# Kernel tuning notes

Hardware: AMD Instinct MI355X
Metric: run time of the kernel (lower is better)

Reference implementation:

```python
import jax, jax.numpy as jnp
import numpy as np

NUM_HEADS = 12
HEAD_DIM = 64
HIDDEN = NUM_HEADS * HEAD_DIM
AGENT_NUM = 40
MAX_POS = 2048
SCALE = HEAD_DIM ** -0.5


def _split_heads(x):
    # [b, s, hidden] -> [b, h, s, d]
    b, s, _ = x.shape
    return x.reshape(b, s, NUM_HEADS, HEAD_DIM).transpose(0, 2, 1, 3)


def _agent_pool(q, agent_num):
    # F.interpolate(q[None], size=(agent_num, dim), mode='bilinear', align_corners=False)
    # width (dim) is unchanged so it reduces to 1D linear interp along seq axis.
    b, s, dim = q.shape
    src = (jnp.arange(agent_num, dtype=q.dtype) + 0.5) * (s / agent_num) - 0.5
    src = jnp.clip(src, 0.0, s - 1.0)
    lo = jnp.floor(src).astype(jnp.int32)
    hi = jnp.minimum(lo + 1, s - 1)
    w = (src - lo.astype(q.dtype))[None, :, None]  # [1, A, 1]
    return q[:, lo, :] * (1.0 - w) + q[:, hi, :] * w  # [b, A, dim]


def setup_inputs() -> dict:
    key = jax.random.key(0)
    ks = jax.random.split(key, 6)
    bs, S = 16, 2048
    return {
        "hidden_states": jax.random.normal(ks[0], (bs, S, HIDDEN), jnp.float32),
        "attention_mask": jnp.zeros((bs, 1, 1, S), jnp.float32),
        "Wq": jax.random.normal(ks[1], (HIDDEN, HIDDEN), jnp.float32) * 0.02,
        "bq": jnp.zeros((HIDDEN,), jnp.float32),
        "Wk": jax.random.normal(ks[2], (HIDDEN, HIDDEN), jnp.float32) * 0.02,
        "bk": jnp.zeros((HIDDEN,), jnp.float32),
        "Wv": jax.random.normal(ks[3], (HIDDEN, HIDDEN), jnp.float32) * 0.02,
        "bv": jnp.zeros((HIDDEN,), jnp.float32),
        "dist_emb": jax.random.normal(ks[4], (2 * MAX_POS - 1, HEAD_DIM), jnp.float32) * 0.02,
    }


def reference(hidden_states, attention_mask, Wq, bq, Wk, bk, Wv, bv, dist_emb):
    bs, S, dim = hidden_states.shape
    q = hidden_states @ Wq + bq          # [b, S, hidden] (== query_layer flattened back)
    k = hidden_states @ Wk + bk
    v = hidden_states @ Wv + bv
    q_layer = _split_heads(q)            # [b, h, S, d]
    k_layer = _split_heads(k)
    v_layer = _split_heads(v)

    agent = _agent_pool(q, AGENT_NUM)    # [b, A, hidden]
    agent_layer = _split_heads(agent)    # [b, h, A, d]

    # stage 1: agent -> KV, with relative-key position bias
    d1 = jnp.arange(AGENT_NUM)[:, None] - jnp.arange(S)[None, :] + (MAX_POS - 1)
    pe1 = dist_emb[d1]                   # [A, S, d]
    bias1 = jnp.einsum('bhad,asd->bhas', agent_layer, pe1)
    score1 = jnp.einsum('bhad,bhsd->bhas', agent_layer * SCALE, k_layer) + bias1
    score1 = score1 + attention_mask     # [b,1,1,S] broadcasts over (h, A)
    p1 = jax.nn.softmax(score1, axis=-1)
    agent_v = jnp.einsum('bhas,bhsd->bhad', p1, v_layer)  # [b, h, A, d]

    # stage 2: query -> agents, with relative-key position bias
    d2 = jnp.arange(S)[:, None] - jnp.arange(AGENT_NUM)[None, :] + (MAX_POS - 1)
    pe2 = dist_emb[d2]                   # [S, A, d]
    bias2 = jnp.einsum('bhsd,sad->bhsa', q_layer, pe2)
    score2 = jnp.einsum('bhsd,bhad->bhsa', q_layer * SCALE, agent_layer) + bias2
    q_mask = jnp.swapaxes(attention_mask, -1, -2)  # [b,1,S,1]
    score2 = score2 + q_mask
    p2 = jax.nn.softmax(score2, axis=-1)
    x = jnp.einsum('bhsa,bhad->bhsd', p2, agent_v)  # [b, h, S, d]
    return x.transpose(0, 2, 1, 3).reshape(bs, S, dim)
```

## Files before the change

kernel.cpp:

```cpp
#include <hip/hip_runtime.h>
#include <math.h>

#define B_ 16
#define S_ 2048
#define H_ 12
#define D_ 64
#define HID 768
#define A_ 40
#define SCALE_ 0.125f
#define CH1 8
#define SUBT 64
#define NSUB 4

typedef __attribute__((ext_vector_type(8))) short short8v;
typedef __attribute__((ext_vector_type(4))) float f32x4;
typedef __attribute__((ext_vector_type(16))) float f32x16;

__device__ __forceinline__ unsigned f2bf_bits(float x) {
    unsigned u = __float_as_uint(x);
    return (u + 0x7FFFu + ((u >> 16) & 1u)) >> 16;
}

__device__ __forceinline__ void split1(float v, unsigned short& h, unsigned short& l) {
    __bf16 bh = (__bf16)v;
    float hf = (float)bh;
    __bf16 bl = (__bf16)(v - hf);
    h = __builtin_bit_cast(unsigned short, bh);
    l = __builtin_bit_cast(unsigned short, bl);
}

__device__ __forceinline__ void split8c(const float* x, int4& hi, int4& lo) {
    unsigned h[8], l[8];
#pragma unroll
    for (int i = 0; i < 8; i++) {
        __bf16 bh = (__bf16)x[i];
        float hf = (float)bh;
        __bf16 bl = (__bf16)(x[i] - hf);
        h[i] = (unsigned)__builtin_bit_cast(unsigned short, bh);
        l[i] = (unsigned)__builtin_bit_cast(unsigned short, bl);
    }
    hi = make_int4((int)(h[0] | (h[1] << 16)), (int)(h[2] | (h[3] << 16)),
                   (int)(h[4] | (h[5] << 16)), (int)(h[6] | (h[7] << 16)));
    lo = make_int4((int)(l[0] | (l[1] << 16)), (int)(l[2] | (l[3] << 16)),
                   (int)(l[4] | (l[5] << 16)), (int)(l[6] | (l[7] << 16)));
}

__global__ void wt_convert(const float* __restrict__ Wq, const float* __restrict__ Wk,
                           const float* __restrict__ Wv,
                           unsigned short* __restrict__ Wth, unsigned short* __restrict__ Wtl)
{
    int idx = blockIdx.x * 256 + threadIdx.x;
    if (idx >= 3 * 192 * 768) return;
    int n  = idx % 768;
    int kc = (idx / 768) % 192;
    int z  = idx / (768 * 192);
    const float* W = (z == 0) ? Wq : (z == 1) ? Wk : Wv;
    unsigned short h4[4], l4[4];
#pragma unroll
    for (int i = 0; i < 4; i++) {
        float x = W[(size_t)(4 * kc + i) * HID + n];
        unsigned hb = f2bf_bits(x);
        float hf = __uint_as_float(hb << 16);
        h4[i] = (unsigned short)hb;
        l4[i] = (unsigned short)f2bf_bits(x - hf);
    }
    size_t o = ((size_t)z * HID + n) * HID + 4 * kc;
    *(ushort4*)&Wth[o] = make_ushort4(h4[0], h4[1], h4[2], h4[3]);
    *(ushort4*)&Wtl[o] = make_ushort4(l4[0], l4[1], l4[2], l4[3]);
}

__global__ void dist_frag(const float* __restrict__ dist,
                          unsigned short* __restrict__ DFh, unsigned short* __restrict__ DFl)
{
    int g = blockIdx.x * 256 + threadIdx.x;
    if (g >= 256 * 2 * 64) return;
    int lane = g & 63;
    int ks = (g >> 6) & 1;
    int u  = g >> 7;
    int row = 8 + u * 16 + (lane & 15);
    int col = ks * 32 + ((lane >> 4) << 3);
    float xv[8];
#pragma unroll
    for (int j = 0; j < 8; j++)
        xv[j] = (row < 4095) ? dist[(size_t)row * D_ + col + j] : 0.f;
    int4 hi, lo;
    split8c(xv, hi, lo);
    *(int4*)&DFh[(size_t)g * 8] = hi;
    *(int4*)&DFl[(size_t)g * 8] = lo;
}

__global__ void ag_frag(const float* __restrict__ Ag,
                        unsigned short* __restrict__ Gh, unsigned short* __restrict__ Gl)
{
    int g = blockIdx.x * 256 + threadIdx.x;
    if (g >= 192 * 3 * 2 * 64) return;
    int lane = g & 63;
    int r = g >> 6;
    int ks = r & 1; r >>= 1;
    int at = r % 3;
    int bh = r / 3;
    int a = at * 16 + (lane & 15);
    int col = ks * 32 + ((lane >> 4) << 3);
    float xv[8];
#pragma unroll
    for (int j = 0; j < 8; j++)
        xv[j] = (a < A_) ? SCALE_ * Ag[((size_t)bh * A_ + a) * D_ + col + j] : 0.f;
    int4 hi, lo;
    split8c(xv, hi, lo);
    *(int4*)&Gh[(size_t)g * 8] = hi;
    *(int4*)&Gl[(size_t)g * 8] = lo;
}

__global__ void avt_frag(const float* __restrict__ AgV,
                         unsigned short* __restrict__ Vh, unsigned short* __restrict__ Vl)
{
    int g = blockIdx.x * 256 + threadIdx.x;
    if (g >= 192 * 4 * 2 * 64) return;
    int lane = g & 63;
    int r = g >> 6;
    int ks = r & 1; r >>= 1;
    int nt = r & 3;
    int bh = r >> 2;
    int d = nt * 16 + (lane & 15);
    int a0 = ks * 32 + ((lane >> 4) << 3);
    float xv[8];
#pragma unroll
    for (int j = 0; j < 8; j++) {
        int a = a0 + j;
        xv[j] = (a < A_) ? AgV[((size_t)bh * A_ + a) * D_ + d] : 0.f;
    }
    int4 hi, lo;
    split8c(xv, hi, lo);
    *(int4*)&Vh[(size_t)g * 8] = hi;
    *(int4*)&Vl[(size_t)g * 8] = lo;
}

__global__ __launch_bounds__(512, 2) void qkv_z(
    const float* __restrict__ X,
    const unsigned short* __restrict__ Wth, const unsigned short* __restrict__ Wtl,
    const float* __restrict__ bq, const float* __restrict__ bk, const float* __restrict__ bv,
    float* __restrict__ Q, float* __restrict__ K, float* __restrict__ V)
{
    const int L   = blockIdx.x;
    const int k8  = L & 7, sl_ = L >> 3;
    const int mt  = k8 * 32 + sl_ / 9;
    const int sub = sl_ % 9;
    const int nt  = sub % 3, zz = sub / 3;
    const int m0 = mt * 128, n0 = nt * 256;

    const float* __restrict__ bias = (zz == 0) ? bq : (zz == 1) ? bk : bv;
    float* __restrict__ Out        = (zz == 0) ? Q  : (zz == 1) ? K  : V;
    const unsigned short* __restrict__ Bhg = Wth + (size_t)zz * HID * HID;
    const unsigned short* __restrict__ Blg = Wtl + (size_t)zz * HID * HID;

    __shared__ unsigned short Ah[128][40];
    __shared__ unsigned short Al[128][40];
    __shared__ unsigned short Bh[256][40];
    __shared__ unsigned short Bl[256][40];

    const int t = threadIdx.x;
    const int lane = t & 63, w = t >> 6;
    const int wm = (w & 1) * 64, wn = (w >> 1) * 64;
    const int r32 = lane & 31, kh = lane >> 5;

    const int sr = t >> 2, sca = (t & 3) * 8;
    const int sb = t >> 1, scb = (t & 1) * 16;

    f32x16 acc[2][2];
#pragma unroll
    for (int i = 0; i < 2; i++)
#pragma unroll
        for (int j = 0; j < 2; j++)
#pragma unroll
            for (int p = 0; p < 16; p++) acc[i][j][p] = 0.f;

    for (int k0 = 0; k0 < HID; k0 += 32) {
        float xv[8];
        const float* xp = X + (size_t)(m0 + sr) * HID + k0 + sca;
        float4 f0 = *(const float4*)xp;
        float4 f1 = *(const float4*)(xp + 4);
        xv[0] = f0.x; xv[1] = f0.y; xv[2] = f0.z; xv[3] = f0.w;
        xv[4] = f1.x; xv[5] = f1.y; xv[6] = f1.z; xv[7] = f1.w;
        int4 ah, al;
        split8c(xv, ah, al);
        size_t bo = (size_t)(n0 + sb) * HID + k0 + scb;
        int4 bh0 = *(const int4*)&Bhg[bo];
        int4 bh1 = *(const int4*)&Bhg[bo + 8];
        int4 bl0 = *(const int4*)&Blg[bo];
        int4 bl1 = *(const int4*)&Blg[bo + 8];

        __syncthreads();
        *(int4*)&Ah[sr][sca] = ah;
        *(int4*)&Al[sr][sca] = al;
        *(int4*)&Bh[sb][scb]     = bh0;  *(int4*)&Bh[sb][scb + 8] = bh1;
        *(int4*)&Bl[sb][scb]     = bl0;  *(int4*)&Bl[sb][scb + 8] = bl1;
        __syncthreads();

#pragma unroll
        for (int ks = 0; ks < 2; ks++) {
            const int ko = ks * 16 + kh * 8;
            short8v a_h[2], a_l[2], b_h[2], b_l[2];
#pragma unroll
            for (int i = 0; i < 2; i++) {
                a_h[i] = *(const short8v*)&Ah[wm + i * 32 + r32][ko];
                a_l[i] = *(const short8v*)&Al[wm + i * 32 + r32][ko];
                b_h[i] = *(const short8v*)&Bh[wn + i * 32 + r32][ko];
                b_l[i] = *(const short8v*)&Bl[wn + i * 32 + r32][ko];
            }
#pragma unroll
            for (int i = 0; i < 2; i++)
#pragma unroll
                for (int j = 0; j < 2; j++) {
                    acc[i][j] = __builtin_amdgcn_mfma_f32_32x32x16_bf16(a_h[i], b_h[j], acc[i][j], 0, 0, 0);
                    acc[i][j] = __builtin_amdgcn_mfma_f32_32x32x16_bf16(a_l[i], b_h[j], acc[i][j], 0, 0, 0);
                    acc[i][j] = __builtin_amdgcn_mfma_f32_32x32x16_bf16(a_h[i], b_l[j], acc[i][j], 0, 0, 0);
                }
        }
    }

    const float scl = (zz == 1) ? SCALE_ : 1.0f;
#pragma unroll
    for (int j = 0; j < 2; j++) {
        int n = n0 + wn + j * 32 + r32;
        float bj = bias[n];
        int h = n >> 6, d = n & 63;
#pragma unroll
        for (int i = 0; i < 2; i++) {
#pragma unroll
            for (int p = 0; p < 16; p++) {
                int m = m0 + wm + i * 32 + (p & 3) + 8 * (p >> 2) + 4 * kh;
                int b = m >> 11, s = m & 2047;
                Out[(((size_t)b * H_ + h) * S_ + s) * D_ + d] = (acc[i][j][p] + bj) * scl;
            }
        }
    }
}

__global__ void agent_pool(const float* __restrict__ Q, float* __restrict__ Ag)
{
    int idx = blockIdx.x * 256 + threadIdx.x;
    if (idx >= B_ * H_ * A_ * D_) return;
    int d  = idx & 63;
    int a  = (idx >> 6) % A_;
    int bh = idx / (A_ * D_);
    float src = ((float)a + 0.5f) * (2048.0f / 40.0f) - 0.5f;
    src = fminf(fmaxf(src, 0.0f), 2047.0f);
    int lo = (int)floorf(src);
    int hi = min(lo + 1, S_ - 1);
    float w = src - (float)lo;
    const float* base = Q + (size_t)bh * (S_ * D_);
    Ag[idx] = base[lo * D_ + d] * (1.0f - w) + base[hi * D_ + d] * w;
}

__global__ __launch_bounds__(256, 3) void stage1_part(
    const float* __restrict__ Kl, const float* __restrict__ Vl,
    const float* __restrict__ Ag, const float* __restrict__ dist,
    const float* __restrict__ mask,
    float* __restrict__ Pacc, float* __restrict__ Pm, float* __restrict__ Pl)
{
    const int q  = blockIdx.x;
    const int bh = blockIdx.y;
    const int b  = bh / H_;
    const int s0 = q * (NSUB * SUBT);
    const float* __restrict__ kb = Kl + (size_t)bh * (S_ * D_);
    const float* __restrict__ vb = Vl + (size_t)bh * (S_ * D_);

    __shared__ float ag[A_][D_];
    __shared__ float pv[103 * 68];
    __shared__ float sc[SUBT][44];
    __shared__ float pm6[6][A_];
    __shared__ float mrow[A_], lrow[A_], resc[A_];

    const int t  = threadIdx.x;
    const int sl = t >> 2, dq = t & 3;

    for (int i = t; i < A_ * D_ / 4; i += 256)
        ((float4*)ag)[i] = ((const float4*)(Ag + (size_t)bh * (A_ * D_)))[i];
    if (t < A_) { mrow[t] = -INFINITY; lrow[t] = 0.0f; }

    float4 acc[3];
#pragma unroll
    for (int ii = 0; ii < 3; ii++) acc[ii] = make_float4(0.f, 0.f, 0.f, 0.f);

    for (int st = 0; st < NSUB; st++) {
        const int sb = s0 + st * SUBT;
        const int jbase = 1984 - sb;

        __syncthreads();
        for (int i = t; i < 103 * 16; i += 256) {
            int r = i >> 4, c = i & 15;
            *(float4*)&pv[r * 68 + c * 4] = *(const float4*)&dist[(size_t)(jbase + r) * D_ + c * 4];
        }
        const int s = sb + sl;
        float4 kreg[4];
        const float* kp = kb + (size_t)s * D_ + dq * 16;
#pragma unroll
        for (int c = 0; c < 4; c++) kreg[c] = *(const float4*)(kp + 4 * c);
        float mval = mask[(size_t)b * S_ + s];
        __syncthreads();

        for (int a = 0; a < A_; a++) {
            const float* per = &pv[(a + 63 - sl) * 68 + dq * 16];
            const float* agr = &ag[a][dq * 16];
            float sum = 0.0f;
#pragma unroll
            for (int c = 0; c < 4; c++) {
                float4 p4 = *(const float4*)(per + 4 * c);
                float4 a4 = *(const float4*)(agr + 4 * c);
                float4 k4 = kreg[c];
                sum = fmaf(a4.x, k4.x + p4.x, sum);
                sum = fmaf(a4.y, k4.y + p4.y, sum);
                sum = fmaf(a4.z, k4.z + p4.z, sum);
                sum = fmaf(a4.w, k4.w + p4.w, sum);
            }
            sum += __shfl_xor(sum, 1);
            sum += __shfl_xor(sum, 2);
            if (dq == 0) sc[sl][a] = sum + mval;
        }
        __syncthreads();

        for (int i = t; i < SUBT * 16; i += 256) {
            int r = i >> 4, c = i & 15;
            *(float4*)&pv[r * 68 + c * 4] = *(const float4*)&vb[(size_t)(sb + r) * D_ + c * 4];
        }
        if (t < 240) {
            int a = t % 40, r6 = t / 40;
            float mx = -INFINITY;
            for (int i = r6; i < SUBT; i += 6) mx = fmaxf(mx, sc[i][a]);
            pm6[r6][a] = mx;
        }
        __syncthreads();
        if (t < A_) {
            float lm = pm6[0][t];
#pragma unroll
            for (int r6 = 1; r6 < 6; r6++) lm = fmaxf(lm, pm6[r6][t]);
            float mnew = fmaxf(mrow[t], lm);
            resc[t] = __expf(mrow[t] - mnew);
            mrow[t] = mnew;
        }
        __syncthreads();
        for (int i = t; i < SUBT * A_; i += 256) {
            int rr = i / 40, aa = i - rr * 40;
            sc[rr][aa] = __expf(sc[rr][aa] - mrow[aa]);
        }
        __syncthreads();
        if (t < 240) {
            int a = t % 40, r6 = t / 40;
            float sm = 0.0f;
            for (int i = r6; i < SUBT; i += 6) sm += sc[i][a];
            pm6[r6][a] = sm;
        }
        __syncthreads();
        if (t < A_) {
            float ls = pm6[0][t] + pm6[1][t] + pm6[2][t] + pm6[3][t] + pm6[4][t] + pm6[5][t];
            lrow[t] = lrow[t] * resc[t] + ls;
        }

#pragma unroll
        for (int ii = 0; ii < 3; ii++) {
            int i = t + ii * 256;
            if (i < A_ * 16) {
                int a = i >> 4, d4 = i & 15;
                float rs = resc[a];
                float4 c4 = acc[ii];
                c4.x *= rs; c4.y *= rs; c4.z *= rs; c4.w *= rs;
                for (int rr = 0; rr < SUBT; rr++) {
                    float p = sc[rr][a];
                    float4 v4 = *(const float4*)&pv[rr * 68 + d4 * 4];
                    c4.x = fmaf(p, v4.x, c4.x);
                    c4.y = fmaf(p, v4.y, c4.y);
                    c4.z = fmaf(p, v4.z, c4.z);
                    c4.w = fmaf(p, v4.w, c4.w);
                }
                acc[ii] = c4;
            }
        }
    }
    __syncthreads();
#pragma unroll
    for (int ii = 0; ii < 3; ii++) {
        int i = t + ii * 256;
        if (i < A_ * 16) {
            int a = i >> 4, d4 = i & 15;
            *(float4*)&Pacc[(((size_t)(bh * CH1 + q) * A_) + a) * D_ + d4 * 4] = acc[ii];
        }
    }
    if (t < A_) {
        Pm[(size_t)(bh * CH1 + q) * A_ + t] = mrow[t];
        Pl[(size_t)(bh * CH1 + q) * A_ + t] = lrow[t];
    }
}

__global__ __launch_bounds__(256) void stage1_reduce(
    const float* __restrict__ Pacc, const float* __restrict__ Pm,
    const float* __restrict__ Pl, float* __restrict__ AgV)
{
    const int bh = blockIdx.x;
    const int t = threadIdx.x;
    __shared__ float F[CH1][A_], Linv[A_];
    if (t < A_) {
        float M = -INFINITY;
#pragma unroll
        for (int q = 0; q < CH1; q++) M = fmaxf(M, Pm[(size_t)(bh * CH1 + q) * A_ + t]);
        float L = 0.0f;
#pragma unroll
        for (int q = 0; q < CH1; q++) {
            float f = __expf(Pm[(size_t)(bh * CH1 + q) * A_ + t] - M);
            F[q][t] = f;
            L = fmaf(f, Pl[(size_t)(bh * CH1 + q) * A_ + t], L);
        }
        Linv[t] = 1.0f / L;
    }
    __syncthreads();
#pragma unroll
    for (int ii = 0; ii < 3; ii++) {
        int i = t + ii * 256;
        if (i < A_ * 16) {
            int a = i >> 4, d4 = i & 15;
            float4 s4 = make_float4(0.f, 0.f, 0.f, 0.f);
            for (int q = 0; q < CH1; q++) {
                float f = F[q][a];
                float4 p4 = *(const float4*)&Pacc[(((size_t)(bh * CH1 + q) * A_) + a) * D_ + d4 * 4];
                s4.x = fmaf(f, p4.x, s4.x);
                s4.y = fmaf(f, p4.y, s4.y);
                s4.z = fmaf(f, p4.z, s4.z);
                s4.w = fmaf(f, p4.w, s4.w);
            }
            float inv = Linv[a];
            s4.x *= inv; s4.y *= inv; s4.z *= inv; s4.w *= inv;
            *(float4*)&AgV[(size_t)bh * (A_ * D_) + a * D_ + d4 * 4] = s4;
        }
    }
}

__global__ __launch_bounds__(256, 2) void stage2_mfma(
    const float* __restrict__ Qg,
    const unsigned short* __restrict__ AGFh, const unsigned short* __restrict__ AGFl,
    const unsigned short* __restrict__ DFh,  const unsigned short* __restrict__ DFl,
    const unsigned short* __restrict__ AVFh, const unsigned short* __restrict__ AVFl,
    float* __restrict__ Out)
{
    const int sbk = blockIdx.x;
    const int bh  = blockIdx.y;
    const int b = bh / H_, h = bh % H_;
    const int s0 = sbk * 64;
    const int base_u = 4 * sbk + 125;

    __shared__ unsigned short Qfh[8 * 64 * 8], Qfl[8 * 64 * 8];
    __shared__ float scm[64][52];
    __shared__ float scp[64][68];
    __shared__ unsigned short PAh[64][72], PAl[64][72];

    const int t = threadIdx.x;
    const int lane = t & 63, ts = t >> 6;
    const int fr = lane & 15, kg = lane >> 4;

    {
        const int r = t >> 2, c0 = (t & 3) * 16;
        const float* qp = Qg + ((size_t)bh * S_ + s0 + r) * D_ + c0;
        float xa[8], xb[8];
        float4 f0 = *(const float4*)(qp);
        float4 f1 = *(const float4*)(qp + 4);
        float4 f2 = *(const float4*)(qp + 8);
        float4 f3 = *(const float4*)(qp + 12);
        xa[0]=f0.x; xa[1]=f0.y; xa[2]=f0.z; xa[3]=f0.w;
        xa[4]=f1.x; xa[5]=f1.y; xa[6]=f1.z; xa[7]=f1.w;
        xb[0]=f2.x; xb[1]=f2.y; xb[2]=f2.z; xb[3]=f2.w;
        xb[4]=f3.x; xb[5]=f3.y; xb[6]=f3.z; xb[7]=f3.w;
        int4 h0, l0, h1, l1;
        split8c(xa, h0, l0);
        split8c(xb, h1, l1);
        const int tsr = r >> 4, frr = r & 15;
        const int c8a = (t & 3) * 2, c8b = c8a + 1;
        const int oa = ((tsr * 2 + (c8a >> 2)) * 64 + (((c8a & 3) << 4) | frr)) * 8;
        const int ob = ((tsr * 2 + (c8b >> 2)) * 64 + (((c8b & 3) << 4) | frr)) * 8;
        *(int4*)&Qfh[oa] = h0;  *(int4*)&Qfl[oa] = l0;
        *(int4*)&Qfh[ob] = h1;  *(int4*)&Qfl[ob] = l1;
    }
    __syncthreads();

    short8v qh[2], ql[2];
#pragma unroll
    for (int ks = 0; ks < 2; ks++) {
        qh[ks] = *(const short8v*)&Qfh[((ts * 2 + ks) * 64 + lane) * 8];
        ql[ks] = *(const short8v*)&Qfl[((ts * 2 + ks) * 64 + lane) * 8];
    }

#pragma unroll
    for (int at = 0; at < 3; at++) {
        f32x4 acc = (f32x4){0.f, 0.f, 0.f, 0.f};
#pragma unroll
        for (int ks = 0; ks < 2; ks++) {
            size_t o = ((((size_t)bh * 3 + at) * 2 + ks) * 64 + lane) * 8;
            short8v chv = *(const short8v*)&AGFh[o];
            short8v clv = *(const short8v*)&AGFl[o];
            acc = __builtin_amdgcn_mfma_f32_16x16x32_bf16(chv, qh[ks], acc, 0, 0, 0);
            acc = __builtin_amdgcn_mfma_f32_16x16x32_bf16(clv, qh[ks], acc, 0, 0, 0);
            acc = __builtin_amdgcn_mfma_f32_16x16x32_bf16(chv, ql[ks], acc, 0, 0, 0);
        }
        *(f32x4*)&scm[ts * 16 + fr][at * 16 + kg * 4] = acc;
    }
#pragma unroll
    for (int o4 = 0; o4 < 4; o4++) {
        f32x4 acc = (f32x4){0.f, 0.f, 0.f, 0.f};
        const int u = base_u + ts + o4;
#pragma unroll
        for (int ks = 0; ks < 2; ks++) {
            size_t o = (((size_t)u * 2 + ks) * 64 + lane) * 8;
            short8v chv = *(const short8v*)&DFh[o];
            short8v clv = *(const short8v*)&DFl[o];
            acc = __builtin_amdgcn_mfma_f32_16x16x32_bf16(chv, qh[ks], acc, 0, 0, 0);
            acc = __builtin_amdgcn_mfma_f32_16x16x32_bf16(clv, qh[ks], acc, 0, 0, 0);
            acc = __builtin_amdgcn_mfma_f32_16x16x32_bf16(chv, ql[ks], acc, 0, 0, 0);
        }
        *(f32x4*)&scp[ts * 16 + fr][o4 * 16 + kg * 4] = acc;
    }
    __syncthreads();

    {
        const int r = t >> 2, dq = t & 3;
        const int base = (r & 15) + 39;
        float val[10];
#pragma unroll
        for (int i = 0; i < 10; i++) {
            int a = dq * 10 + i;
            val[i] = scm[r][a] + scp[r][base - a];
        }
        float mx = -INFINITY;
#pragma unroll
        for (int i = 0; i < 10; i++) mx = fmaxf(mx, val[i]);
        mx = fmaxf(mx, __shfl_xor(mx, 1));
        mx = fmaxf(mx, __shfl_xor(mx, 2));
        float sum = 0.f;
#pragma unroll
        for (int i = 0; i < 10; i++) { val[i] = __expf(val[i] - mx); sum += val[i]; }
        sum += __shfl_xor(sum, 1);
        sum += __shfl_xor(sum, 2);
        float inv = 1.0f / sum;
        unsigned* ph = (unsigned*)&PAh[r][0];
        unsigned* pl = (unsigned*)&PAl[r][0];
#pragma unroll
        for (int i = 0; i < 5; i++) {
            unsigned short h0, l0, h1, l1;
            split1(val[2 * i] * inv, h0, l0);
            split1(val[2 * i + 1] * inv, h1, l1);
            ph[dq * 5 + i] = (unsigned)h0 | ((unsigned)h1 << 16);
            pl[dq * 5 + i] = (unsigned)l0 | ((unsigned)l1 << 16);
        }
#pragma unroll
        for (int i = 0; i < 3; i++) { ph[20 + dq * 3 + i] = 0u; pl[20 + dq * 3 + i] = 0u; }
    }
    __syncthreads();

    short8v ph8[2], pl8[2];
#pragma unroll
    for (int ks = 0; ks < 2; ks++) {
        ph8[ks] = *(const short8v*)&PAh[ts * 16 + fr][ks * 32 + kg * 8];
        pl8[ks] = *(const short8v*)&PAl[ts * 16 + fr][ks * 32 + kg * 8];
    }
#pragma unroll
    for (int nt = 0; nt < 4; nt++) {
        f32x4 acc = (f32x4){0.f, 0.f, 0.f, 0.f};
#pragma unroll
        for (int ks = 0; ks < 2; ks++) {
            size_t o = ((((size_t)bh * 4 + nt) * 2 + ks) * 64 + lane) * 8;
            short8v vh = *(const short8v*)&AVFh[o];
            short8v vl = *(const short8v*)&AVFl[o];
            acc = __builtin_amdgcn_mfma_f32_16x16x32_bf16(ph8[ks], vh, acc, 0, 0, 0);
            acc = __builtin_amdgcn_mfma_f32_16x16x32_bf16(pl8[ks], vh, acc, 0, 0, 0);
            acc = __builtin_amdgcn_mfma_f32_16x16x32_bf16(ph8[ks], vl, acc, 0, 0, 0);
        }
        const int d = nt * 16 + fr;
        float* op = Out + ((size_t)b * S_ + s0 + ts * 16 + kg * 4) * HID + h * D_ + d;
#pragma unroll
        for (int r = 0; r < 4; r++)
            op[(size_t)r * HID] = acc[r];
    }
}

extern "C" void kernel_launch(void* const* d_in, const int* in_sizes, int n_in,
                              void* d_out, int out_size, void* d_ws, size_t ws_size,
                              hipStream_t stream) {
    const float* hs   = (const float*)d_in[0];
    const float* mask = (const float*)d_in[1];
    const float* Wq   = (const float*)d_in[2];
    const float* bq   = (const float*)d_in[3];
    const float* Wk   = (const float*)d_in[4];
    const float* bk   = (const float*)d_in[5];
    const float* Wv   = (const float*)d_in[6];
    const float* bv   = (const float*)d_in[7];
    const float* dist = (const float*)d_in[8];
    float* out = (float*)d_out;

    float* ws = (float*)d_ws;
    const size_t QKV = (size_t)B_ * H_ * S_ * D_;
    const size_t AG  = (size_t)B_ * H_ * A_ * D_;
    float* Q     = ws;
    float* K     = ws + QKV;
    float* V     = ws + 2 * QKV;
    float* Agent = ws + 3 * QKV;
    float* AgV   = Agent + AG;
    float* Pacc  = AgV + AG;
    float* Pm    = Pacc + (size_t)B_ * H_ * CH1 * A_ * D_;
    float* Pl    = Pm + (size_t)B_ * H_ * CH1 * A_;
    unsigned short* Wth = (unsigned short*)(Pl + (size_t)B_ * H_ * CH1 * A_);
    unsigned short* Wtl = Wth + (size_t)3 * HID * HID;
    unsigned short* DFh = Wtl + (size_t)3 * HID * HID;
    unsigned short* DFl = DFh + (size_t)262144;
    unsigned short* AGFh = DFl + (size_t)262144;
    unsigned short* AGFl = AGFh + (size_t)589824;
    unsigned short* AVFh = AGFl + (size_t)589824;
    unsigned short* AVFl = AVFh + (size_t)786432;

    wt_convert<<<(3 * 192 * 768 + 255) / 256, 256, 0, stream>>>(Wq, Wk, Wv, Wth, Wtl);
    dist_frag<<<(256 * 2 * 64 + 255) / 256, 256, 0, stream>>>(dist, DFh, DFl);
    qkv_z<<<2304, 512, 0, stream>>>(hs, Wth, Wtl, bq, bk, bv, Q, K, V);
    agent_pool<<<(B_ * H_ * A_ * D_ + 255) / 256, 256, 0, stream>>>(Q, Agent);
    ag_frag<<<(192 * 3 * 2 * 64 + 255) / 256, 256, 0, stream>>>(Agent, AGFh, AGFl);
    dim3 g1(CH1, B_ * H_);
    stage1_part<<<g1, 256, 0, stream>>>(K, V, Agent, dist, mask, Pacc, Pm, Pl);
    stage1_reduce<<<B_ * H_, 256, 0, stream>>>(Pacc, Pm, Pl, AgV);
    avt_frag<<<(192 * 4 * 2 * 64 + 255) / 256, 256, 0, stream>>>(AgV, AVFh, AVFl);
    dim3 g2(32, B_ * H_);
    stage2_mfma<<<g2, 256, 0, stream>>>(Q, AGFh, AGFl, DFh, DFl, AVFh, AVFl, out);
}
```

Before: 654.4 us.

## Move stage-1 agent attention onto bf16x3 MFMA with split QK and position-bias GEMMs

Rewrites the stage-1 kernel so the agent·K score, the agent·dist_emb position bias, and the P·V accumulation all run on 16x16x32 bf16 MFMA using a hi/lo split (three products) to keep near-fp32 accuracy. The position bias is computed as a small dense GEMM over a 112-row band of dist_emb and then diagonally gathered, instead of per-element dot products. New fragment-conversion kernels (dist_frag0, an unscaled ag_frag) are launched and K/V tiles are converted to bf16 fragments in shared memory each subtile. This adds conversion overhead, more shared memory and lower occupancy (launch bound 2) in exchange for replacing scalar FMA loops with matrix instructions.

```diff
diff --git a/kernel.cpp b/kernel.cpp
--- a/kernel.cpp
+++ b/kernel.cpp
@@ -89,8 +89,28 @@
     *(int4*)&DFl[(size_t)g * 8] = lo;
 }
 
+__global__ void dist_frag0(const float* __restrict__ dist,
+                           unsigned short* __restrict__ Dh, unsigned short* __restrict__ Dl)
+{
+    int g = blockIdx.x * 256 + threadIdx.x;
+    if (g >= 131 * 2 * 64) return;
+    int lane = g & 63;
+    int ks = (g >> 6) & 1;
+    int u  = g >> 7;
+    int row = u * 16 + (lane & 15);
+    int col = ks * 32 + ((lane >> 4) << 3);
+    float xv[8];
+#pragma unroll
+    for (int j = 0; j < 8; j++) xv[j] = dist[(size_t)row * D_ + col + j];
+    int4 hi, lo;
+    split8c(xv, hi, lo);
+    *(int4*)&Dh[(size_t)g * 8] = hi;
+    *(int4*)&Dl[(size_t)g * 8] = lo;
+}
+
 __global__ void ag_frag(const float* __restrict__ Ag,
-                        unsigned short* __restrict__ Gh, unsigned short* __restrict__ Gl)
+                        unsigned short* __restrict__ Gh, unsigned short* __restrict__ Gl,
+                        float scale)
 {
     int g = blockIdx.x * 256 + threadIdx.x;
     if (g >= 192 * 3 * 2 * 64) return;
@@ -104,7 +124,7 @@
     float xv[8];
 #pragma unroll
     for (int j = 0; j < 8; j++)
-        xv[j] = (a < A_) ? SCALE_ * Ag[((size_t)bh * A_ + a) * D_ + col + j] : 0.f;
+        xv[j] = (a < A_) ? scale * Ag[((size_t)bh * A_ + a) * D_ + col + j] : 0.f;
     int4 hi, lo;
     split8c(xv, hi, lo);
     *(int4*)&Gh[(size_t)g * 8] = hi;
@@ -252,9 +272,10 @@
     Ag[idx] = base[lo * D_ + d] * (1.0f - w) + base[hi * D_ + d] * w;
 }
 
-__global__ __launch_bounds__(256, 3) void stage1_part(
+__global__ __launch_bounds__(256, 2) void stage1_mfma(
     const float* __restrict__ Kl, const float* __restrict__ Vl,
-    const float* __restrict__ Ag, const float* __restrict__ dist,
+    const unsigned short* __restrict__ AG1h, const unsigned short* __restrict__ AG1l,
+    const unsigned short* __restrict__ D0h,  const unsigned short* __restrict__ D0l,
     const float* __restrict__ mask,
     float* __restrict__ Pacc, float* __restrict__ Pm, float* __restrict__ Pl)
 {
@@ -265,64 +286,122 @@
     const float* __restrict__ kb = Kl + (size_t)bh * (S_ * D_);
     const float* __restrict__ vb = Vl + (size_t)bh * (S_ * D_);
 
-    __shared__ float ag[A_][D_];
-    __shared__ float pv[103 * 68];
-    __shared__ float sc[SUBT][44];
+    __shared__ unsigned short KFh[4096], KFl[4096];
+    __shared__ unsigned short VTh[4096], VTl[4096];
+    __shared__ float sc[SUBT][52];
+    __shared__ float scp[112][52];
     __shared__ float pm6[6][A_];
-    __shared__ float mrow[A_], lrow[A_], resc[A_];
-
-    const int t  = threadIdx.x;
-    const int sl = t >> 2, dq = t & 3;
-
-    for (int i = t; i < A_ * D_ / 4; i += 256)
-        ((float4*)ag)[i] = ((const float4*)(Ag + (size_t)bh * (A_ * D_)))[i];
+    __shared__ float mrow[A_], lrow[A_], resc[A_], mrw[SUBT];
+
+    const int t = threadIdx.x;
+    const int lane = t & 63, w = t >> 6;
+    const int fr = lane & 15, kg = lane >> 4;
+
     if (t < A_) { mrow[t] = -INFINITY; lrow[t] = 0.0f; }
 
-    float4 acc[3];
-#pragma unroll
-    for (int ii = 0; ii < 3; ii++) acc[ii] = make_float4(0.f, 0.f, 0.f, 0.f);
+    f32x4 acc3[3];
+#pragma unroll
+    for (int at = 0; at < 3; at++) acc3[at] = (f32x4){0.f, 0.f, 0.f, 0.f};
 
     for (int st = 0; st < NSUB; st++) {
         const int sb = s0 + st * SUBT;
-        const int jbase = 1984 - sb;
-
-        __syncthreads();
-        for (int i = t; i < 103 * 16; i += 256) {
-            int r = i >> 4, c = i & 15;
-            *(float4*)&pv[r * 68 + c * 4] = *(const float4*)&dist[(size_t)(jbase + r) * D_ + c * 4];
-        }
-        const int s = sb + sl;
-        float4 kreg[4];
-        const float* kp = kb + (size_t)s * D_ + dq * 16;
-#pragma unroll
-        for (int c = 0; c < 4; c++) kreg[c] = *(const float4*)(kp + 4 * c);
-        float mval = mask[(size_t)b * S_ + s];
-        __syncthreads();
-
-        for (int a = 0; a < A_; a++) {
-            const float* per = &pv[(a + 63 - sl) * 68 + dq * 16];
-            const float* agr = &ag[a][dq * 16];
-            float sum = 0.0f;
-#pragma unroll
-            for (int c = 0; c < 4; c++) {
-                float4 p4 = *(const float4*)(per + 4 * c);
-                float4 a4 = *(const float4*)(agr + 4 * c);
-                float4 k4 = kreg[c];
-                sum = fmaf(a4.x, k4.x + p4.x, sum);
-                sum = fmaf(a4.y, k4.y + p4.y, sum);
-                sum = fmaf(a4.z, k4.z + p4.z, sum);
-                sum = fmaf(a4.w, k4.w + p4.w, sum);
+        const int u0 = (1984 - sb) >> 4;
+
+        __syncthreads();
+
+        {
+            const int r = t >> 2, c0 = (t & 3) * 16;
+            const float* kp = kb + (size_t)(sb + r) * D_ + c0;
+            float xa[8], xb[8];
+            float4 f0 = *(const float4*)(kp);
+            float4 f1 = *(const float4*)(kp + 4);
+            float4 f2 = *(const float4*)(kp + 8);
+            float4 f3 = *(const float4*)(kp + 12);
+            xa[0]=f0.x; xa[1]=f0.y; xa[2]=f0.z; xa[3]=f0.w;
+            xa[4]=f1.x; xa[5]=f1.y; xa[6]=f1.z; xa[7]=f1.w;
+            xb[0]=f2.x; xb[1]=f2.y; xb[2]=f2.z; xb[3]=f2.w;
+            xb[4]=f3.x; xb[5]=f3.y; xb[6]=f3.z; xb[7]=f3.w;
+            int4 h0, l0, h1, l1;
+            split8c(xa, h0, l0);
+            split8c(xb, h1, l1);
+            const int tsr = r >> 4, frr = r & 15;
+            const int c8a = (t & 3) * 2, c8b = c8a + 1;
+            const int oa = ((tsr * 2 + (c8a >> 2)) * 64 + (((c8a & 3) << 4) | frr)) * 8;
+            const int ob = ((tsr * 2 + (c8b >> 2)) * 64 + (((c8b & 3) << 4) | frr)) * 8;
+            *(int4*)&KFh[oa] = h0;  *(int4*)&KFl[oa] = l0;
+            *(int4*)&KFh[ob] = h1;  *(int4*)&KFl[ob] = l1;
+        }
+        {
+            const int r = t >> 2, c0 = (t & 3) * 16;
+            const float* vp = vb + (size_t)(sb + r) * D_ + c0;
+            float vv[16];
+            float4 g0 = *(const float4*)(vp);
+            float4 g1 = *(const float4*)(vp + 4);
+            float4 g2 = *(const float4*)(vp + 8);
+            float4 g3 = *(const float4*)(vp + 12);
+            vv[0]=g0.x; vv[1]=g0.y; vv[2]=g0.z; vv[3]=g0.w;
+            vv[4]=g1.x; vv[5]=g1.y; vv[6]=g1.z; vv[7]=g1.w;
+            vv[8]=g2.x; vv[9]=g2.y; vv[10]=g2.z; vv[11]=g2.w;
+            vv[12]=g3.x; vv[13]=g3.y; vv[14]=g3.z; vv[15]=g3.w;
+            const int ks2 = r >> 5, kgp = (r & 31) >> 3, e = r & 7;
+#pragma unroll
+            for (int jj = 0; jj < 16; jj++) {
+                int d = c0 + jj;
+                int off = (((d >> 4) * 2 + ks2) * 64 + kgp * 16 + (d & 15)) * 8 + e;
+                unsigned short h, l;
+                split1(vv[jj], h, l);
+                VTh[off] = h; VTl[off] = l;
             }
-            sum += __shfl_xor(sum, 1);
-            sum += __shfl_xor(sum, 2);
-            if (dq == 0) sc[sl][a] = sum + mval;
-        }
-        __syncthreads();
-
-        for (int i = t; i < SUBT * 16; i += 256) {
-            int r = i >> 4, c = i & 15;
-            *(float4*)&pv[r * 68 + c * 4] = *(const float4*)&vb[(size_t)(sb + r) * D_ + c * 4];
-        }
+        }
+        if (t < SUBT) mrw[t] = mask[(size_t)b * S_ + sb + t];
+        __syncthreads();
+
+        {
+            const int ts = w;
+#pragma unroll
+            for (int at = 0; at < 3; at++) {
+                f32x4 a4 = (f32x4){0.f, 0.f, 0.f, 0.f};
+#pragma unroll
+                for (int ks = 0; ks < 2; ks++) {
+                    size_t oA = ((((size_t)bh * 3 + at) * 2 + ks) * 64 + lane) * 8;
+                    short8v gh = *(const short8v*)&AG1h[oA];
+                    short8v gl = *(const short8v*)&AG1l[oA];
+                    short8v kh2 = *(const short8v*)&KFh[((ts * 2 + ks) * 64 + lane) * 8];
+                    short8v kl2 = *(const short8v*)&KFl[((ts * 2 + ks) * 64 + lane) * 8];
+                    a4 = __builtin_amdgcn_mfma_f32_16x16x32_bf16(gh, kh2, a4, 0, 0, 0);
+                    a4 = __builtin_amdgcn_mfma_f32_16x16x32_bf16(gl, kh2, a4, 0, 0, 0);
+                    a4 = __builtin_amdgcn_mfma_f32_16x16x32_bf16(gh, kl2, a4, 0, 0, 0);
+                }
+                *(f32x4*)&sc[ts * 16 + fr][at * 16 + kg * 4] = a4;
+            }
+        }
+        for (int ut = w; ut < 7; ut += 4) {
+            const int u = u0 + ut;
+#pragma unroll
+            for (int at = 0; at < 3; at++) {
+                f32x4 a4 = (f32x4){0.f, 0.f, 0.f, 0.f};
+#pragma unroll
+                for (int ks = 0; ks < 2; ks++) {
+                    size_t oA = ((((size_t)bh * 3 + at) * 2 + ks) * 64 + lane) * 8;
+                    short8v gh = *(const short8v*)&AG1h[oA];
+                    short8v gl = *(const short8v*)&AG1l[oA];
+                    size_t oD = (((size_t)u * 2 + ks) * 64 + lane) * 8;
+                    short8v dh = *(const short8v*)&D0h[oD];
+                    short8v dl = *(const short8v*)&D0l[oD];
+                    a4 = __builtin_amdgcn_mfma_f32_16x16x32_bf16(gh, dh, a4, 0, 0, 0);
+                    a4 = __builtin_amdgcn_mfma_f32_16x16x32_bf16(gl, dh, a4, 0, 0, 0);
+                    a4 = __builtin_amdgcn_mfma_f32_16x16x32_bf16(gh, dl, a4, 0, 0, 0);
+                }
+                *(f32x4*)&scp[ut * 16 + fr][at * 16 + kg * 4] = a4;
+            }
+        }
+        __syncthreads();
+
+        for (int i = t; i < SUBT * A_; i += 256) {
+            int rr = i / 40, aa = i - rr * 40;
+            sc[rr][aa] += scp[aa + 63 - rr][aa] + mrw[rr];
+        }
+        __syncthreads();
         if (t < 240) {
             int a = t % 40, r6 = t / 40;
             float mx = -INFINITY;
@@ -355,34 +434,62 @@
             float ls = pm6[0][t] + pm6[1][t] + pm6[2][t] + pm6[3][t] + pm6[4][t] + pm6[5][t];
             lrow[t] = lrow[t] * resc[t] + ls;
         }
-
-#pragma unroll
-        for (int ii = 0; ii < 3; ii++) {
-            int i = t + ii * 256;
-            if (i < A_ * 16) {
-                int a = i >> 4, d4 = i & 15;
-                float rs = resc[a];
-                float4 c4 = acc[ii];
-                c4.x *= rs; c4.y *= rs; c4.z *= rs; c4.w *= rs;
-                for (int rr = 0; rr < SUBT; rr++) {
-                    float p = sc[rr][a];
-                    float4 v4 = *(const float4*)&pv[rr * 68 + d4 * 4];
-                    c4.x = fmaf(p, v4.x, c4.x);
-                    c4.y = fmaf(p, v4.y, c4.y);
-                    c4.z = fmaf(p, v4.z, c4.z);
-                    c4.w = fmaf(p, v4.w, c4.w);
+        __syncthreads();
+
+        for (int g = t; g < 384; g += 256) {
+            int pl = g & 63;
+            int c = g >> 6;
+            int at = c >> 1, ks2 = c & 1;
+            int a = at * 16 + (pl & 15);
+            int sl0 = ks2 * 32 + (pl >> 4) * 8;
+            float xv[8];
+#pragma unroll
+            for (int e = 0; e < 8; e++)
+                xv[e] = (a < A_) ? sc[sl0 + e][a] : 0.f;
+            int4 hi, lo;
+            split8c(xv, hi, lo);
+            *(int4*)&KFh[g * 8] = hi;
+            *(int4*)&KFl[g * 8] = lo;
+        }
+        __syncthreads();
+
+        {
+            const int dt = w;
+#pragma unroll
+            for (int at = 0; at < 3; at++) {
+                f32x4 a4 = acc3[at];
+#pragma unroll
+                for (int p = 0; p < 4; p++) {
+                    int a = at * 16 + kg * 4 + p;
+                    float rs = (a < A_) ? resc[a] : 0.f;
+                    a4[p] *= rs;
                 }
-                acc[ii] = c4;
+#pragma unroll
+                for (int ks2 = 0; ks2 < 2; ks2++) {
+                    short8v ph = *(const short8v*)&KFh[((at * 2 + ks2) * 64 + lane) * 8];
+                    short8v pll = *(const short8v*)&KFl[((at * 2 + ks2) * 64 + lane) * 8];
+                    short8v vh = *(const short8v*)&VTh[((dt * 2 + ks2) * 64 + lane) * 8];
+                    short8v vl = *(const short8v*)&VTl[((dt * 2 + ks2) * 64 + lane) * 8];
+                    a4 = __builtin_amdgcn_mfma_f32_16x16x32_bf16(ph, vh, a4, 0, 0, 0);
+                    a4 = __builtin_amdgcn_mfma_f32_16x16x32_bf16(pll, vh, a4, 0, 0, 0);
+                    a4 = __builtin_amdgcn_mfma_f32_16x16x32_bf16(ph, vl, a4, 0, 0, 0);
+                }
+                acc3[at] = a4;
             }
         }
     }
     __syncthreads();
-#pragma unroll
-    for (int ii = 0; ii < 3; ii++) {
-        int i = t + ii * 256;
-        if (i < A_ * 16) {
-            int a = i >> 4, d4 = i & 15;
-            *(float4*)&Pacc[(((size_t)(bh * CH1 + q) * A_) + a) * D_ + d4 * 4] = acc[ii];
+
+    {
+        const int dt = w;
+#pragma unroll
+        for (int at = 0; at < 3; at++) {
+#pragma unroll
+            for (int p = 0; p < 4; p++) {
+                int a = at * 16 + kg * 4 + p;
+                if (a < A_)
+                    Pacc[(((size_t)(bh * CH1 + q) * A_) + a) * D_ + dt * 16 + fr] = acc3[at][p];
+            }
         }
     }
     if (t < A_) {
@@ -611,14 +718,20 @@
     unsigned short* AGFl = AGFh + (size_t)589824;
     unsigned short* AVFh = AGFl + (size_t)589824;
     unsigned short* AVFl = AVFh + (size_t)786432;
+    unsigned short* AG1h = AVFl + (size_t)786432;
+    unsigned short* AG1l = AG1h + (size_t)589824;
+    unsigned short* D0h  = AG1l + (size_t)589824;
+    unsigned short* D0l  = D0h + (size_t)134144;
 
     wt_convert<<<(3 * 192 * 768 + 255) / 256, 256, 0, stream>>>(Wq, Wk, Wv, Wth, Wtl);
     dist_frag<<<(256 * 2 * 64 + 255) / 256, 256, 0, stream>>>(dist, DFh, DFl);
+    dist_frag0<<<(131 * 2 * 64 + 255) / 256, 256, 0, stream>>>(dist, D0h, D0l);
     qkv_z<<<2304, 512, 0, stream>>>(hs, Wth, Wtl, bq, bk, bv, Q, K, V);
     agent_pool<<<(B_ * H_ * A_ * D_ + 255) / 256, 256, 0, stream>>>(Q, Agent);
-    ag_frag<<<(192 * 3 * 2 * 64 + 255) / 256, 256, 0, stream>>>(Agent, AGFh, AGFl);
+    ag_frag<<<(192 * 3 * 2 * 64 + 255) / 256, 256, 0, stream>>>(Agent, AGFh, AGFl, SCALE_);
+    ag_frag<<<(192 * 3 * 2 * 64 + 255) / 256, 256, 0, stream>>>(Agent, AG1h, AG1l, 1.0f);
     dim3 g1(CH1, B_ * H_);
-    stage1_part<<<g1, 256, 0, stream>>>(K, V, Agent, dist, mask, Pacc, Pm, Pl);
+    stage1_mfma<<<g1, 256, 0, stream>>>(K, V, AG1h, AG1l, D0h, D0l, mask, Pacc, Pm, Pl);
     stage1_reduce<<<B_ * H_, 256, 0, stream>>>(Pacc, Pm, Pl, AgV);
     avt_frag<<<(192 * 4 * 2 * 64 + 255) / 256, 256, 0, stream>>>(AgV, AVFh, AVFl);
     dim3 g2(32, B_ * H_);
```

Result: faster. 578.5 us (-11.6%).
